# Optimization experiments

Measured on AMD Instinct MI355X. Metric: run time of the kernel, lower is better.

Reference implementation:

```python
import jax, jax.numpy as jnp
from jax import lax
import numpy as np

B, S, T, R = 64, 50, 50, 2   # batch, n_prev_sents, n_words, n_responses
V, H = 32000, 256            # vocab, hidden (= emb_size)


def gru_scan(xs, h0, Wih, Whh, bih, bhh):
    """Torch-style GRU over xs [T, N, I]; returns (outs [T,N,H], h_last [N,H])."""
    gi_all = jnp.einsum('tni,gi->tng', xs, Wih) + bih  # input gates precomputed
    def step(h, gi):
        gh = h @ Whh.T + bhh
        ir, iz, inn = jnp.split(gi, 3, -1)
        hr, hz, hn = jnp.split(gh, 3, -1)
        r = jax.nn.sigmoid(ir + hr)
        z = jax.nn.sigmoid(iz + hz)
        n = jnp.tanh(inn + r * hn)
        h = (1.0 - z) * n + z * h
        return h, h
    h_last, outs = lax.scan(step, h0, gi_all)
    return outs, h_last


def agent_tables():
    # replicates get_agent_emb: np.random.seed(1), one fresh uniform table per batch
    np.random.seed(1)
    return jnp.asarray(np.stack([np.random.uniform(0, 1, (S + 1, H)) for _ in range(B)]).astype(np.float32))


def setup_inputs() -> dict:
    key = jax.random.key(0)
    ks = jax.random.split(key, 24)
    k = 1.0 / np.sqrt(H)
    u = lambda kk, shape: jax.random.uniform(kk, shape, jnp.float32, -k, k)
    inp = {
        'context': jax.random.randint(ks[0], (B, S, T), 0, V, jnp.int32),
        'response': jax.random.randint(ks[1], (B, R, T), 0, V, jnp.int32),
        'spk_agents': jax.random.randint(ks[2], (B, S), 0, S + 1, jnp.int32),
        'emb_utter': jax.random.normal(ks[3], (V, H), jnp.float32) * 0.1,
        'emb_resp': jax.random.normal(ks[4], (V, H), jnp.float32) * 0.1,
        'utter_Wih': u(ks[5], (3 * H, H)), 'utter_Whh': u(ks[6], (3 * H, H)),
        'utter_bih': u(ks[7], (3 * H,)), 'utter_bhh': u(ks[8], (3 * H,)),
        'ctx_Wih': u(ks[9], (3 * H, 2 * H)), 'ctx_Whh': u(ks[10], (3 * H, H)),
        'ctx_bih': u(ks[11], (3 * H,)), 'ctx_bhh': u(ks[12], (3 * H,)),
        'resp_Wih': u(ks[13], (3 * H, H)), 'resp_Whh': u(ks[14], (3 * H, H)),
        'resp_bih': u(ks[15], (3 * H,)), 'resp_bhh': u(ks[16], (3 * H,)),
        'spk_Wih': u(ks[17], (3 * H, H)), 'spk_Whh': u(ks[18], (3 * H, H)),
        'spk_bih': u(ks[19], (3 * H,)), 'spk_bhh': u(ks[20], (3 * H,)),
    }
    return inp


def forward(context, response, spk_agents, emb_utter, emb_resp,
            utter_Wih, utter_Whh, utter_bih, utter_bhh,
            ctx_Wih, ctx_Whh, ctx_bih, ctx_bhh,
            resp_Wih, resp_Whh, resp_bih, resp_bhh,
            spk_Wih, spk_Whh, spk_bih, spk_bhh):
    # ---- utterance encoder: all B*S utterances batched through one GRU ----
    xu = emb_utter[context.reshape(B * S, T)]                 # [B*S, T, H]
    xu = jnp.transpose(xu, (1, 0, 2))                         # [T, B*S, H]
    _, hu = gru_scan(xu, jnp.zeros((B * S, H), jnp.float32),
                     utter_Wih, utter_Whh, utter_bih, utter_bhh)
    utter_hidden = hu.reshape(B, S, H).transpose(1, 0, 2)     # [S, B, H]

    # ---- agent embeddings (per-batch random tables, gathered by speaker id) ----
    tables = agent_tables()                                   # [B, S+1, H] constant
    agent_emb = jnp.take_along_axis(tables, spk_agents[:, :, None].astype(jnp.int32), axis=1)  # [B,S,H]
    agent_emb = jnp.transpose(agent_emb, (1, 0, 2))           # [S, B, H]

    # ---- context GRU over utterances ----
    ctx_in = jnp.concatenate([utter_hidden, agent_emb], axis=2)  # [S, B, 2H]
    context_output, ctx_h = gru_scan(ctx_in, jnp.zeros((B, H), jnp.float32),
                                     ctx_Wih, ctx_Whh, ctx_bih, ctx_bhh)
    context_hidden = ctx_h[None]                              # [1, B, H]

    # ---- speaker encoder: masked GRU == GRU over each speaker's subsequence ----
    sp_ids = jnp.arange(S + 1)
    active = (spk_agents[:, :, None] == sp_ids[None, None, :])  # [B, S, S+1]
    active_t = jnp.transpose(active, (1, 0, 2))                 # [S, B, S+1]
    gi_all = jnp.einsum('sbh,gh->sbg', context_output, spk_Wih) + spk_bih  # [S, B, 3H]

    def spk_step(h, inputs):
        gi, act = inputs                                        # gi [B,3H], act [B,S+1]
        gh = jnp.einsum('bsh,gh->bsg', h, spk_Whh) + spk_bhh    # [B, S+1, 3H]
        ir, iz, inn = jnp.split(gi[:, None, :], 3, -1)
        hr, hz, hn = jnp.split(gh, 3, -1)
        r = jax.nn.sigmoid(ir + hr)
        z = jax.nn.sigmoid(iz + hz)
        n = jnp.tanh(inn + r * hn)
        h_new = (1.0 - z) * n + z * h
        return jnp.where(act[:, :, None], h_new, h), None

    h_spk, _ = lax.scan(spk_step, jnp.zeros((B, S + 1, H), jnp.float32), (gi_all, active_t))
    present = active.any(axis=1)                               # [B, S+1]
    spk_emb = h_spk * present[:, :, None]                      # rows of absent speakers stay 0
    spk_emb_mask = (present & (sp_ids[None, :] > 0)).astype(jnp.float32)  # [B, S+1]

    # ---- response encoder: all B*R responses batched ----
    xr = emb_resp[response.reshape(B * R, T)]                  # [B*R, T, H]
    xr = jnp.transpose(xr, (1, 0, 2))                          # [T, B*R, H]
    outs, hr_ = gru_scan(xr, jnp.zeros((B * R, H), jnp.float32),
                         resp_Wih, resp_Whh, resp_bih, resp_bhh)
    resp_output = outs.reshape(T, B, R, H).transpose(2, 0, 1, 3)  # [R, T, B, H]
    resp_hidden = hr_.reshape(B, R, H).transpose(1, 0, 2)         # [R, B, H]

    return (context_output, context_hidden, resp_output, resp_hidden, spk_emb, spk_emb_mask)


def reference(context, response, spk_agents, emb_utter, emb_resp,
              utter_Wih, utter_Whh, utter_bih, utter_bhh,
              ctx_Wih, ctx_Whh, ctx_bih, ctx_bhh,
              resp_Wih, resp_Whh, resp_bih, resp_bhh,
              spk_Wih, spk_Whh, spk_bih, spk_bhh):
    return forward(context, response, spk_agents, emb_utter, emb_resp,
                   utter_Wih, utter_Whh, utter_bih, utter_bhh,
                   ctx_Wih, ctx_Whh, ctx_bih, ctx_bhh,
                   resp_Wih, resp_Whh, resp_bih, resp_bhh,
                   spk_Wih, spk_Whh, spk_bih, spk_bhh)
```

## Files before the change

kernel.cpp:

```cpp
#include <hip/hip_runtime.h>
#include <hip/hip_bf16.h>
#include <stdint.h>
#include <stdlib.h>
#include <math.h>

typedef __hip_bfloat16 bf16;
typedef unsigned short ushort;
typedef __attribute__((ext_vector_type(8))) short bhalf8;
typedef __attribute__((ext_vector_type(4))) float f32x4;

#define Bn 64
#define Sn 50
#define Tn 50
#define Hn 256

#define OFF_CTX_OUT   0
#define OFF_CTX_HID   819200
#define OFF_RESP_OUT  835584
#define OFF_RESP_HID  2473984
#define OFF_SPK_EMB   2506752
#define OFF_SPK_MASK  3342336

#define WS_FLAG   0u
#define WS_HU     256u
#define WS_REG    1638912u
#define RG_UTTQ   0u
#define RG_UTTSC  24576000u
#define RG_RESPGI 0u
#define RG_CO     9830400u
#define RG_GIC    13107200u
#define RG_GIS    18022400u
#define RG_TBL    22937600u
#define WS_END    26342912u

__device__ __forceinline__ float b2f_bits(unsigned int b) {
    union { unsigned int u; float f; } c; c.u = b; return c.f;
}
__device__ __forceinline__ float bf2f(ushort v) { return b2f_bits(((unsigned int)v) << 16); }
__device__ __forceinline__ ushort f2bf(float f) {
    union { float f; unsigned int u; } c; c.f = f;
    return (ushort)((c.u + 0x7fffu + ((c.u >> 16) & 1u)) >> 16);
}
template<bool BF>
__device__ __forceinline__ bhalf8 ldfrag(const void* __restrict__ p, size_t i) {
    if (BF) {
        return *(const bhalf8*)((const ushort*)p + i);
    } else {
        const float* q = (const float*)p + i;
        float4 a = *(const float4*)q;
        float4 b = *(const float4*)(q + 4);
        bhalf8 r;
        r[0] = (short)f2bf(a.x); r[1] = (short)f2bf(a.y);
        r[2] = (short)f2bf(a.z); r[3] = (short)f2bf(a.w);
        r[4] = (short)f2bf(b.x); r[5] = (short)f2bf(b.y);
        r[6] = (short)f2bf(b.z); r[7] = (short)f2bf(b.w);
        return r;
    }
}
template<bool BF>
__device__ __forceinline__ float ldw(const void* __restrict__ p, int i) {
    return BF ? bf2f(((const ushort*)p)[i]) : ((const float*)p)[i];
}
template<bool BF>
__device__ __forceinline__ void stout(void* __restrict__ out, size_t i, float v) {
    if (BF) ((ushort*)out)[i] = f2bf(v);
    else    ((float*)out)[i] = v;
}
__device__ __forceinline__ float fsigm(float x) {
    return __builtin_amdgcn_rcpf(1.f + __expf(-x));
}
__device__ __forceinline__ float ftanh(float x) {
    float e = __expf(-2.f * x);
    return (1.f - e) * __builtin_amdgcn_rcpf(1.f + e);
}

__global__ void sniff_kernel(const void* __restrict__ w, int* __restrict__ flag) {
    const unsigned int* p = (const unsigned int*)w;
    int tid = threadIdx.x;
    bool big = false;
    for (int i = tid; i < 512; i += 64) {
        float v = b2f_bits(p[i] << 16);
        if (!(fabsf(v) <= 1.0f)) big = true;
    }
    unsigned long long m = __ballot(big);
    if (tid == 0) *flag = (m == 0ull) ? 1 : 0;
}


template<bool BF>
__device__ void vocab_utt_body(
    const void* __restrict__ emb_u, const void* __restrict__ uWih,
    const void* __restrict__ ubih,
    char* __restrict__ Q, float* __restrict__ SC,
    float* bhs, float (*rmx)[16])
{
    const int tid = threadIdx.x;
    const int w = tid >> 6, l = tid & 63, quad = l >> 4, c = l & 15;

    for (int i = tid; i < 768; i += 512) bhs[i] = ldw<BF>(ubih, i);

    bhalf8 wf[3][2][8];
    #pragma unroll
    for (int g = 0; g < 3; ++g)
        #pragma unroll
        for (int ctl = 0; ctl < 2; ++ctl) {
            const int gcol = g * 256 + 32 * w + 16 * ctl + c;
            #pragma unroll
            for (int tk = 0; tk < 8; ++tk)
                wf[g][ctl][tk] = ldfrag<BF>(uWih, (size_t)gcol * 256 + 32 * tk + 8 * quad);
        }
    __syncthreads();

    for (int vt = blockIdx.x; vt < 2000; vt += gridDim.x) {
        f32x4 acc[3][2];
        #pragma unroll
        for (int g = 0; g < 3; ++g)
            #pragma unroll
            for (int ctl = 0; ctl < 2; ++ctl) {
                float b = bhs[g * 256 + 32 * w + 16 * ctl + c];
                acc[g][ctl] = (f32x4){b, b, b, b};
            }
        #pragma unroll
        for (int tk = 0; tk < 8; ++tk) {
            bhalf8 a = ldfrag<BF>(emb_u, (size_t)(vt * 16 + c) * 256 + 32 * tk + 8 * quad);
            #pragma unroll
            for (int g = 0; g < 3; ++g)
                #pragma unroll
                for (int ctl = 0; ctl < 2; ++ctl)
                    acc[g][ctl] = __builtin_amdgcn_mfma_f32_16x16x32_bf16(
                        a, wf[g][ctl][tk], acc[g][ctl], 0, 0, 0);
        }

        float mx[4];
        #pragma unroll
        for (int r = 0; r < 4; ++r) {
            float v = 0.f;
            #pragma unroll
            for (int g = 0; g < 3; ++g)
                #pragma unroll
                for (int ctl = 0; ctl < 2; ++ctl)
                    v = fmaxf(v, fabsf(acc[g][ctl][r]));
            mx[r] = v;
        }
        #pragma unroll
        for (int off = 1; off < 16; off <<= 1)
            #pragma unroll
            for (int r = 0; r < 4; ++r)
                mx[r] = fmaxf(mx[r], __shfl_xor(mx[r], off));
        if (c == 0)
            #pragma unroll
            for (int r = 0; r < 4; ++r) rmx[w][4 * quad + r] = mx[r];
        __syncthreads();

        #pragma unroll
        for (int r = 0; r < 4; ++r) {
            const int m = 4 * quad + r;
            float s = fmaxf(fmaxf(fmaxf(rmx[0][m], rmx[1][m]), fmaxf(rmx[2][m], rmx[3][m])),
                            fmaxf(fmaxf(rmx[4][m], rmx[5][m]), fmaxf(rmx[6][m], rmx[7][m])));
            float scale = s * (1.f / 127.f);
            float inv   = (s > 0.f) ? (127.f / s) : 0.f;
            #pragma unroll
            for (int g = 0; g < 3; ++g)
                #pragma unroll
                for (int ctl = 0; ctl < 2; ++ctl) {
                    int qv = __float2int_rn(acc[g][ctl][r] * inv);
                    qv = max(-127, min(127, qv));
                    Q[(size_t)(vt * 16 + m) * 768 + g * 256 + 32 * w + 16 * ctl + c] = (char)qv;
                }
            if (w == 0 && c == 0) SC[vt * 16 + m] = scale;
        }
        __syncthreads();
    }
}

__global__ __launch_bounds__(512, 1) void vocab_utt_kernel(
    const void* emb_u, const void* uWih, const void* ubih,
    char* Q, float* SC, const int* flag)
{
    __shared__ float bhs[768];
    __shared__ float rmx[8][16];
    if (*flag) vocab_utt_body<true >(emb_u, uWih, ubih, Q, SC, bhs, rmx);
    else       vocab_utt_body<false>(emb_u, uWih, ubih, Q, SC, bhs, rmx);
}

template<bool BF>
__device__ void rec_utt_body(
    const int* __restrict__ ctx_tok,
    const char* __restrict__ Q, const float* __restrict__ SC,
    const void* __restrict__ uWhh, const void* __restrict__ ubhh,
    ushort* __restrict__ H_u,
    char (*gq)[16][784], float (*gsc)[16], ushort (*hb)[16][264])
{
    const int n0 = blockIdx.x * 16;
    const int tid = threadIdx.x;
    const int w = tid >> 6, l = tid & 63, quad = l >> 4, c = l & 15;

    for (int i = tid; i < 16 * 264; i += 512) (&hb[0][0][0])[i] = 0;

    float breg[3][2];
    #pragma unroll
    for (int g = 0; g < 3; ++g)
        #pragma unroll
        for (int ctl = 0; ctl < 2; ++ctl)
            breg[g][ctl] = ldw<BF>(ubhh, g * 256 + 32 * w + 16 * ctl + c);

    bhalf8 wf[3][2][8];
    #pragma unroll
    for (int g = 0; g < 3; ++g)
        #pragma unroll
        for (int ctl = 0; ctl < 2; ++ctl) {
            const int gcol = g * 256 + 32 * w + 16 * ctl + c;
            #pragma unroll
            for (int tk = 0; tk < 8; ++tk)
                wf[g][ctl][tk] = ldfrag<BF>(uWhh, (size_t)gcol * 256 + 32 * tk + 8 * quad);
        }

    float st[2][4];
    #pragma unroll
    for (int ctl = 0; ctl < 2; ++ctl)
        #pragma unroll
        for (int r = 0; r < 4; ++r) st[ctl][r] = 0.f;

    const int pm = tid >> 5, pc = tid & 31;
    uint2 pf[3]; float psc = 0.f;
    {
        const int tok0 = ctx_tok[(n0 + pm) * Tn + 0];
        const char* src = Q + (size_t)tok0 * 768 + pc * 24;
        #pragma unroll
        for (int s = 0; s < 3; ++s) pf[s] = *(const uint2*)(src + s * 8);
        #pragma unroll
        for (int s = 0; s < 3; ++s) *(uint2*)(&gq[0][pm][pc * 24 + s * 8]) = pf[s];
        if (pc == 0) gsc[0][pm] = SC[tok0];
    }
    __syncthreads();

    int p = 0;
    for (int t = 0; t < Tn; ++t) {
        if (t < Tn - 1) {
            const int tok1 = ctx_tok[(n0 + pm) * Tn + t + 1];
            const char* src = Q + (size_t)tok1 * 768 + pc * 24;
            #pragma unroll
            for (int s = 0; s < 3; ++s) pf[s] = *(const uint2*)(src + s * 8);
            if (pc == 0) psc = SC[tok1];
        }

        f32x4 acc[3][2];
        #pragma unroll
        for (int g = 0; g < 3; ++g)
            #pragma unroll
            for (int ctl = 0; ctl < 2; ++ctl) {
                float b = breg[g][ctl];
                acc[g][ctl] = (f32x4){b, b, b, b};
            }
        #pragma unroll
        for (int tk = 0; tk < 8; ++tk) {
            bhalf8 a = *(const bhalf8*)(&hb[p][c][32 * tk + 8 * quad]);
            #pragma unroll
            for (int g = 0; g < 3; ++g)
                #pragma unroll
                for (int ctl = 0; ctl < 2; ++ctl)
                    acc[g][ctl] = __builtin_amdgcn_mfma_f32_16x16x32_bf16(
                        a, wf[g][ctl][tk], acc[g][ctl], 0, 0, 0);
        }

        #pragma unroll
        for (int ctl = 0; ctl < 2; ++ctl) {
            const int u = 32 * w + 16 * ctl + c;
            #pragma unroll
            for (int r = 0; r < 4; ++r) {
                const int m = 4 * quad + r;
                const float s = gsc[p][m];
                float gr = s * (float)(signed char)gq[p][m][u];
                float gz = s * (float)(signed char)gq[p][m][256 + u];
                float gn = s * (float)(signed char)gq[p][m][512 + u];
                float rr = fsigm(gr + acc[0][ctl][r]);
                float zz = fsigm(gz + acc[1][ctl][r]);
                float nn = ftanh(gn + rr * acc[2][ctl][r]);
                float h  = (1.f - zz) * nn + zz * st[ctl][r];
                st[ctl][r] = h;
                hb[p ^ 1][m][u] = f2bf(h);
            }
        }
        if (t < Tn - 1) {
            #pragma unroll
            for (int s = 0; s < 3; ++s) *(uint2*)(&gq[p ^ 1][pm][pc * 24 + s * 8]) = pf[s];
            if (pc == 0) gsc[p ^ 1][pm] = psc;
        }
        __syncthreads();
        p ^= 1;
    }

    #pragma unroll
    for (int ctl = 0; ctl < 2; ++ctl)
        #pragma unroll
        for (int r = 0; r < 4; ++r)
            H_u[(size_t)(n0 + 4 * quad + r) * Hn + 32 * w + 16 * ctl + c] = f2bf(st[ctl][r]);
}

__global__ __launch_bounds__(512, 1) void rec_utt_kernel(
    const int* ctx_tok, const char* Q, const float* SC,
    const void* uWhh, const void* ubhh, ushort* H_u, const int* flag)
{
    __shared__ char   gq[2][16][784];
    __shared__ float  gsc[2][16];
    __shared__ ushort hb[2][16][264];
    if (*flag) rec_utt_body<true >(ctx_tok, Q, SC, uWhh, ubhh, H_u, gq, gsc, hb);
    else       rec_utt_body<false>(ctx_tok, Q, SC, uWhh, ubhh, H_u, gq, gsc, hb);
}

template<bool BF>
__device__ void respgi_body(
    int bid,
    const int* __restrict__ rsp_tok, const void* __restrict__ emb_r,
    const void* __restrict__ rWih, const void* __restrict__ rbih,
    ushort* __restrict__ RG, float* bhs)
{
    const int tid = threadIdx.x;
    const int w = tid >> 6, l = tid & 63, quad = l >> 4, c = l & 15;

    for (int i = tid; i < 768; i += 512) bhs[i] = ldw<BF>(rbih, i);

    bhalf8 wf[3][2][8];
    #pragma unroll
    for (int g = 0; g < 3; ++g)
        #pragma unroll
        for (int ctl = 0; ctl < 2; ++ctl) {
            const int gcol = g * 256 + 32 * w + 16 * ctl + c;
            #pragma unroll
            for (int tk = 0; tk < 8; ++tk)
                wf[g][ctl][tk] = ldfrag<BF>(rWih, (size_t)gcol * 256 + 32 * tk + 8 * quad);
        }
    __syncthreads();

    const int inst = bid * 16 + c;
    const int tok  = rsp_tok[inst];

    f32x4 acc[3][2];
    #pragma unroll
    for (int g = 0; g < 3; ++g)
        #pragma unroll
        for (int ctl = 0; ctl < 2; ++ctl) {
            float b = bhs[g * 256 + 32 * w + 16 * ctl + c];
            acc[g][ctl] = (f32x4){b, b, b, b};
        }
    #pragma unroll
    for (int tk = 0; tk < 8; ++tk) {
        bhalf8 a = ldfrag<BF>(emb_r, (size_t)tok * 256 + 32 * tk + 8 * quad);
        #pragma unroll
        for (int g = 0; g < 3; ++g)
            #pragma unroll
            for (int ctl = 0; ctl < 2; ++ctl)
                acc[g][ctl] = __builtin_amdgcn_mfma_f32_16x16x32_bf16(
                    a, wf[g][ctl][tk], acc[g][ctl], 0, 0, 0);
    }
    #pragma unroll
    for (int g = 0; g < 3; ++g)
        #pragma unroll
        for (int ctl = 0; ctl < 2; ++ctl)
            #pragma unroll
            for (int r = 0; r < 4; ++r)
                RG[(size_t)(bid * 16 + 4 * quad + r) * 768
                   + g * 256 + 32 * w + 16 * ctl + c] = f2bf(acc[g][ctl][r]);
}

template<bool BF>
__device__ void rec_resp_body(
    int bid,
    const ushort* __restrict__ RG,
    const void* __restrict__ rWhh, const void* __restrict__ rbhh,
    void* __restrict__ outp,
    ushort (*gx)[16][776], ushort (*hb)[16][264])
{
    const int n0 = bid * 16;
    const int tid = threadIdx.x;
    const int w = tid >> 6, l = tid & 63, quad = l >> 4, c = l & 15;

    for (int i = tid; i < 16 * 264; i += 512) (&hb[0][0][0])[i] = 0;

    float breg[3][2];
    #pragma unroll
    for (int g = 0; g < 3; ++g)
        #pragma unroll
        for (int ctl = 0; ctl < 2; ++ctl)
            breg[g][ctl] = ldw<BF>(rbhh, g * 256 + 32 * w + 16 * ctl + c);

    bhalf8 wf[3][2][8];
    #pragma unroll
    for (int g = 0; g < 3; ++g)
        #pragma unroll
        for (int ctl = 0; ctl < 2; ++ctl) {
            const int gcol = g * 256 + 32 * w + 16 * ctl + c;
            #pragma unroll
            for (int tk = 0; tk < 8; ++tk)
                wf[g][ctl][tk] = ldfrag<BF>(rWhh, (size_t)gcol * 256 + 32 * tk + 8 * quad);
        }

    float st[2][4];
    #pragma unroll
    for (int ctl = 0; ctl < 2; ++ctl)
        #pragma unroll
        for (int r = 0; r < 4; ++r) st[ctl][r] = 0.f;

    const int pm = tid >> 5, pc = tid & 31;
    uint4 pf[3];
    {
        const ushort* src = RG + (size_t)((n0 + pm) * Tn + 0) * 768 + pc * 24;
        #pragma unroll
        for (int s = 0; s < 3; ++s) pf[s] = *(const uint4*)(src + s * 8);
        #pragma unroll
        for (int s = 0; s < 3; ++s) *(uint4*)(&gx[0][pm][pc * 24 + s * 8]) = pf[s];
    }
    __syncthreads();

    int p = 0;
    for (int t = 0; t < Tn; ++t) {
        if (t > 0) {
            #pragma unroll
            for (int ctl = 0; ctl < 2; ++ctl) {
                const int u = 32 * w + 16 * ctl + c;
                #pragma unroll
                for (int r = 0; r < 4; ++r) {
                    const int n = n0 + 4 * quad + r, bb = n >> 1, ri = n & 1;
                    stout<BF>(outp, OFF_RESP_OUT
                              + (size_t)((ri * Tn + (t - 1)) * Bn + bb) * Hn + u,
                              st[ctl][r]);
                }
            }
        }
        if (t < Tn - 1) {
            const ushort* src = RG + (size_t)((n0 + pm) * Tn + t + 1) * 768 + pc * 24;
            #pragma unroll
            for (int s = 0; s < 3; ++s) pf[s] = *(const uint4*)(src + s * 8);
        }

        f32x4 acc[3][2];
        #pragma unroll
        for (int g = 0; g < 3; ++g)
            #pragma unroll
            for (int ctl = 0; ctl < 2; ++ctl) {
                float b = breg[g][ctl];
                acc[g][ctl] = (f32x4){b, b, b, b};
            }
        #pragma unroll
        for (int tk = 0; tk < 8; ++tk) {
            bhalf8 a = *(const bhalf8*)(&hb[p][c][32 * tk + 8 * quad]);
            #pragma unroll
            for (int g = 0; g < 3; ++g)
                #pragma unroll
                for (int ctl = 0; ctl < 2; ++ctl)
                    acc[g][ctl] = __builtin_amdgcn_mfma_f32_16x16x32_bf16(
                        a, wf[g][ctl][tk], acc[g][ctl], 0, 0, 0);
        }

        #pragma unroll
        for (int ctl = 0; ctl < 2; ++ctl) {
            const int u = 32 * w + 16 * ctl + c;
            #pragma unroll
            for (int r = 0; r < 4; ++r) {
                const int m = 4 * quad + r;
                float gr = bf2f(gx[p][m][u]);
                float gz = bf2f(gx[p][m][256 + u]);
                float gn = bf2f(gx[p][m][512 + u]);
                float rr = fsigm(gr + acc[0][ctl][r]);
                float zz = fsigm(gz + acc[1][ctl][r]);
                float nn = ftanh(gn + rr * acc[2][ctl][r]);
                float h  = (1.f - zz) * nn + zz * st[ctl][r];
                st[ctl][r] = h;
                hb[p ^ 1][m][u] = f2bf(h);
            }
        }
        if (t < Tn - 1) {
            #pragma unroll
            for (int s = 0; s < 3; ++s) *(uint4*)(&gx[p ^ 1][pm][pc * 24 + s * 8]) = pf[s];
        }
        __syncthreads();
        p ^= 1;
    }

    #pragma unroll
    for (int ctl = 0; ctl < 2; ++ctl) {
        const int u = 32 * w + 16 * ctl + c;
        #pragma unroll
        for (int r = 0; r < 4; ++r) {
            const int n = n0 + 4 * quad + r, bb = n >> 1, ri = n & 1;
            stout<BF>(outp, OFF_RESP_OUT
                      + (size_t)((ri * Tn + (Tn - 1)) * Bn + bb) * Hn + u, st[ctl][r]);
            stout<BF>(outp, OFF_RESP_HID + (size_t)(ri * Bn + bb) * Hn + u, st[ctl][r]);
        }
    }
}

template<bool BF>
__device__ void gi_ctx_body(
    int bid,
    const ushort* __restrict__ H_u, const ushort* __restrict__ tblbf,
    const int* __restrict__ spk_agents,
    const void* __restrict__ Wih, const void* __restrict__ bih,
    ushort* __restrict__ GIc, float* bhs)
{
    const int tid = threadIdx.x;
    const int w = tid >> 6, l = tid & 63, quad = l >> 4, c = l & 15;

    for (int i = tid; i < 768; i += 512) bhs[i] = ldw<BF>(bih, i);
    __syncthreads();

    const int m0 = bid * 16;
    const int m  = m0 + c, s = m >> 6, b = m & 63;
    const int a  = spk_agents[b * Sn + s];
    const ushort* arow0 = H_u   + (size_t)(b * Sn + s) * Hn;
    const ushort* arow1 = tblbf + (size_t)(b * 51 + a) * Hn;

    f32x4 acc[3][2];
    #pragma unroll
    for (int g = 0; g < 3; ++g)
        #pragma unroll
        for (int ctl = 0; ctl < 2; ++ctl) {
            float bb = bhs[g * 256 + 32 * w + 16 * ctl + c];
            acc[g][ctl] = (f32x4){bb, bb, bb, bb};
        }

    for (int half = 0; half < 2; ++half) {
        const ushort* ar = half ? arow1 : arow0;
        bhalf8 af[8];
        #pragma unroll
        for (int tk = 0; tk < 8; ++tk)
            af[tk] = *(const bhalf8*)(ar + 32 * tk + 8 * quad);
        #pragma unroll
        for (int g = 0; g < 3; ++g) {
            bhalf8 wf[2][8];
            #pragma unroll
            for (int ctl = 0; ctl < 2; ++ctl) {
                const int gcol = g * 256 + 32 * w + 16 * ctl + c;
                #pragma unroll
                for (int tk = 0; tk < 8; ++tk)
                    wf[ctl][tk] = ldfrag<BF>(Wih,
                        (size_t)gcol * 512 + half * 256 + 32 * tk + 8 * quad);
            }
            #pragma unroll
            for (int tk = 0; tk < 8; ++tk)
                #pragma unroll
                for (int ctl = 0; ctl < 2; ++ctl)
                    acc[g][ctl] = __builtin_amdgcn_mfma_f32_16x16x32_bf16(
                        af[tk], wf[ctl][tk], acc[g][ctl], 0, 0, 0);
        }
    }

    #pragma unroll
    for (int g = 0; g < 3; ++g)
        #pragma unroll
        for (int ctl = 0; ctl < 2; ++ctl)
            #pragma unroll
            for (int r = 0; r < 4; ++r)
                GIc[(size_t)(m0 + 4 * quad + r) * 768
                    + g * 256 + 32 * w + 16 * ctl + c] = f2bf(acc[g][ctl][r]);
}

__global__ __launch_bounds__(512, 1) void gates2_kernel(
    const int* rsp_tok, const void* emb_r, const void* rWih, const void* rbih,
    ushort* RG,
    const ushort* H_u, const ushort* tblbf, const int* spk_agents,
    const void* cWih, const void* cbih, ushort* GIc, const int* flag)
{
    __shared__ float bhs[768];
    if (blockIdx.x < 400) {
        if (*flag) respgi_body<true >(blockIdx.x, rsp_tok, emb_r, rWih, rbih, RG, bhs);
        else       respgi_body<false>(blockIdx.x, rsp_tok, emb_r, rWih, rbih, RG, bhs);
    } else {
        const int bid = blockIdx.x - 400;
        if (*flag) gi_ctx_body<true >(bid, H_u, tblbf, spk_agents, cWih, cbih, GIc, bhs);
        else       gi_ctx_body<false>(bid, H_u, tblbf, spk_agents, cWih, cbih, GIc, bhs);
    }
}

template<bool BF>
__device__ void ctx_rec_body(
    int bid,
    const ushort* __restrict__ GIc,
    const void* __restrict__ Whh, const void* __restrict__ bhh,
    float* __restrict__ CO, void* __restrict__ outp,
    ushort (*gx)[16][776], ushort (*hb)[16][264])
{
    const int n0 = bid * 16;
    const int tid = threadIdx.x;
    const int w = tid >> 6, l = tid & 63, quad = l >> 4, c = l & 15;

    for (int i = tid; i < 16 * 264; i += 512) (&hb[0][0][0])[i] = 0;

    float breg[3][2];
    #pragma unroll
    for (int g = 0; g < 3; ++g)
        #pragma unroll
        for (int ctl = 0; ctl < 2; ++ctl)
            breg[g][ctl] = ldw<BF>(bhh, g * 256 + 32 * w + 16 * ctl + c);

    bhalf8 wf[3][2][8];
    #pragma unroll
    for (int g = 0; g < 3; ++g)
        #pragma unroll
        for (int ctl = 0; ctl < 2; ++ctl) {
            const int gcol = g * 256 + 32 * w + 16 * ctl + c;
            #pragma unroll
            for (int tk = 0; tk < 8; ++tk)
                wf[g][ctl][tk] = ldfrag<BF>(Whh, (size_t)gcol * 256 + 32 * tk + 8 * quad);
        }

    float st[2][4];
    #pragma unroll
    for (int ctl = 0; ctl < 2; ++ctl)
        #pragma unroll
        for (int r = 0; r < 4; ++r) st[ctl][r] = 0.f;

    const int pm = tid >> 5, pc = tid & 31;
    uint4 pf[3];
    {
        const ushort* src = GIc + (size_t)(0 * Bn + n0 + pm) * 768 + pc * 24;
        #pragma unroll
        for (int s = 0; s < 3; ++s) pf[s] = *(const uint4*)(src + s * 8);
        #pragma unroll
        for (int s = 0; s < 3; ++s) *(uint4*)(&gx[0][pm][pc * 24 + s * 8]) = pf[s];
    }
    __syncthreads();

    int p = 0;
    for (int t = 0; t < Sn; ++t) {
        if (t > 0) {
            #pragma unroll
            for (int ctl = 0; ctl < 2; ++ctl) {
                const int u = 32 * w + 16 * ctl + c;
                #pragma unroll
                for (int r = 0; r < 4; ++r) {
                    const size_t gri = (size_t)((t - 1) * Bn + n0 + 4 * quad + r);
                    CO[gri * Hn + u] = st[ctl][r];
                    stout<BF>(outp, OFF_CTX_OUT + gri * Hn + u, st[ctl][r]);
                }
            }
        }
        if (t < Sn - 1) {
            const ushort* src = GIc + (size_t)((t + 1) * Bn + n0 + pm) * 768 + pc * 24;
            #pragma unroll
            for (int s = 0; s < 3; ++s) pf[s] = *(const uint4*)(src + s * 8);
        }

        f32x4 acc[3][2];
        #pragma unroll
        for (int g = 0; g < 3; ++g)
            #pragma unroll
            for (int ctl = 0; ctl < 2; ++ctl) {
                float b = breg[g][ctl];
                acc[g][ctl] = (f32x4){b, b, b, b};
            }
        #pragma unroll
        for (int tk = 0; tk < 8; ++tk) {
            bhalf8 a = *(const bhalf8*)(&hb[p][c][32 * tk + 8 * quad]);
            #pragma unroll
            for (int g = 0; g < 3; ++g)
                #pragma unroll
                for (int ctl = 0; ctl < 2; ++ctl)
                    acc[g][ctl] = __builtin_amdgcn_mfma_f32_16x16x32_bf16(
                        a, wf[g][ctl][tk], acc[g][ctl], 0, 0, 0);
        }

        #pragma unroll
        for (int ctl = 0; ctl < 2; ++ctl) {
            const int u = 32 * w + 16 * ctl + c;
            #pragma unroll
            for (int r = 0; r < 4; ++r) {
                const int m = 4 * quad + r;
                float gr = bf2f(gx[p][m][u]);
                float gz = bf2f(gx[p][m][256 + u]);
                float gn = bf2f(gx[p][m][512 + u]);
                float rr = fsigm(gr + acc[0][ctl][r]);
                float zz = fsigm(gz + acc[1][ctl][r]);
                float nn = ftanh(gn + rr * acc[2][ctl][r]);
                float h  = (1.f - zz) * nn + zz * st[ctl][r];
                st[ctl][r] = h;
                hb[p ^ 1][m][u] = f2bf(h);
            }
        }
        if (t < Sn - 1) {
            #pragma unroll
            for (int s = 0; s < 3; ++s) *(uint4*)(&gx[p ^ 1][pm][pc * 24 + s * 8]) = pf[s];
        }
        __syncthreads();
        p ^= 1;
    }

    #pragma unroll
    for (int ctl = 0; ctl < 2; ++ctl) {
        const int u = 32 * w + 16 * ctl + c;
        #pragma unroll
        for (int r = 0; r < 4; ++r) {
            const int m = 4 * quad + r;
            const size_t gri = (size_t)((Sn - 1) * Bn + n0 + m);
            CO[gri * Hn + u] = st[ctl][r];
            stout<BF>(outp, OFF_CTX_OUT + gri * Hn + u, st[ctl][r]);
            stout<BF>(outp, OFF_CTX_HID + (size_t)(n0 + m) * Hn + u, st[ctl][r]);
        }
    }
}

__global__ __launch_bounds__(512, 1) void rec2_kernel(
    const ushort* GIc, const void* cWhh, const void* cbhh, float* CO,
    const ushort* RG, const void* rWhh, const void* rbhh,
    void* outp, const int* flag)
{
    __shared__ ushort gx[2][16][776];
    __shared__ ushort hb[2][16][264];
    if (blockIdx.x < 4) {
        if (*flag) ctx_rec_body<true >(blockIdx.x, GIc, cWhh, cbhh, CO, outp, gx, hb);
        else       ctx_rec_body<false>(blockIdx.x, GIc, cWhh, cbhh, CO, outp, gx, hb);
    } else {
        const int bid = blockIdx.x - 4;
        if (*flag) rec_resp_body<true >(bid, RG, rWhh, rbhh, outp, gx, hb);
        else       rec_resp_body<false>(bid, RG, rWhh, rbhh, outp, gx, hb);
    }
}

template<bool BF>
__device__ void gi_spk_body(
    const float* __restrict__ CO,
    const void* __restrict__ Wih, const void* __restrict__ bih,
    ushort* __restrict__ GIs, float* bhs)
{
    const int tid = threadIdx.x;
    const int w = tid >> 6, l = tid & 63, quad = l >> 4, c = l & 15;

    for (int i = tid; i < 768; i += 512) bhs[i] = ldw<BF>(bih, i);

    bhalf8 wf[3][2][8];
    #pragma unroll
    for (int g = 0; g < 3; ++g)
        #pragma unroll
        for (int ctl = 0; ctl < 2; ++ctl) {
            const int gcol = g * 256 + 32 * w + 16 * ctl + c;
            #pragma unroll
            for (int tk = 0; tk < 8; ++tk)
                wf[g][ctl][tk] = ldfrag<BF>(Wih, (size_t)gcol * 256 + 32 * tk + 8 * quad);
        }
    __syncthreads();

    f32x4 acc[3][2];
    #pragma unroll
    for (int g = 0; g < 3; ++g)
        #pragma unroll
        for (int ctl = 0; ctl < 2; ++ctl) {
            float b = bhs[g * 256 + 32 * w + 16 * ctl + c];
            acc[g][ctl] = (f32x4){b, b, b, b};
        }
    #pragma unroll
    for (int tk = 0; tk < 8; ++tk) {
        bhalf8 a = ldfrag<false>(CO, (size_t)(blockIdx.x * 16 + c) * 256 + 32 * tk + 8 * quad);
        #pragma unroll
        for (int g = 0; g < 3; ++g)
            #pragma unroll
            for (int ctl = 0; ctl < 2; ++ctl)
                acc[g][ctl] = __builtin_amdgcn_mfma_f32_16x16x32_bf16(
                    a, wf[g][ctl][tk], acc[g][ctl], 0, 0, 0);
    }
    #pragma unroll
    for (int g = 0; g < 3; ++g)
        #pragma unroll
        for (int ctl = 0; ctl < 2; ++ctl)
            #pragma unroll
            for (int r = 0; r < 4; ++r)
                GIs[(size_t)(blockIdx.x * 16 + 4 * quad + r) * 768
                    + g * 256 + 32 * w + 16 * ctl + c] = f2bf(acc[g][ctl][r]);
}

__global__ __launch_bounds__(512, 1) void gi_spk_kernel(
    const float* CO, const void* Wih, const void* bih, ushort* GIs, const int* flag)
{
    __shared__ float bhs[768];
    if (*flag) gi_spk_body<true >(CO, Wih, bih, GIs, bhs);
    else       gi_spk_body<false>(CO, Wih, bih, GIs, bhs);
}

#define SSTR 264
template<bool BF>
__device__ void spk_rec_body(
    const ushort* __restrict__ GIs,
    const void* __restrict__ Whh, const void* __restrict__ bhh,
    const int* __restrict__ spk_agents,
    void* __restrict__ outp,
    ushort* S , ushort (*gx)[776], int* pres , float* bhs)
{
    const int b0 = blockIdx.x * 4;
    const int tid = threadIdx.x;
    const int w = tid >> 6, l = tid & 63, quad = l >> 4, c = l & 15;

    for (int i = tid; i < 768; i += 512) bhs[i] = ldw<BF>(bhh, i);
    for (int i = tid; i < 4 * 51 * SSTR; i += 512) S[i] = 0;
    for (int i = tid; i < 4 * 51; i += 512) pres[i] = 0;

    bhalf8 wf[3][2][8];
    #pragma unroll
    for (int g = 0; g < 3; ++g)
        #pragma unroll
        for (int ctl = 0; ctl < 2; ++ctl) {
            const int gcol = g * 256 + 32 * w + 16 * ctl + c;
            #pragma unroll
            for (int tk = 0; tk < 8; ++tk)
                wf[g][ctl][tk] = ldfrag<BF>(Whh, (size_t)gcol * 256 + 32 * tk + 8 * quad);
        }

    const int prow = (tid & 255) >> 6;
    const int pseg = tid & 63;
    uint2 pf[3];
    if (tid < 256) {
        const ushort* src = GIs + (size_t)(0 * Bn + b0 + prow) * 768 + pseg * 12;
        #pragma unroll
        for (int s = 0; s < 3; ++s) pf[s] = *(const uint2*)(src + s * 4);
        #pragma unroll
        for (int s = 0; s < 3; ++s) *(uint2*)(&gx[prow][pseg * 12 + s * 4]) = pf[s];
    }
    __syncthreads();

    for (int t = 0; t < Sn; ++t) {
        const int va = (c < 4) ? spk_agents[(b0 + c) * Sn + t] : 0;
        const int mb = (c < 4) ? c : 0;

        if (tid < 256 && t < Sn - 1) {
            const ushort* src = GIs + (size_t)((t + 1) * Bn + b0 + prow) * 768 + pseg * 12;
            #pragma unroll
            for (int s = 0; s < 3; ++s) pf[s] = *(const uint2*)(src + s * 4);
        }

        f32x4 acc[3][2];
        #pragma unroll
        for (int g = 0; g < 3; ++g)
            #pragma unroll
            for (int ctl = 0; ctl < 2; ++ctl) {
                float b = bhs[g * 256 + 32 * w + 16 * ctl + c];
                acc[g][ctl] = (f32x4){b, b, b, b};
            }
        const ushort* srow = &S[(mb * 51 + va) * SSTR];
        #pragma unroll
        for (int tk = 0; tk < 8; ++tk) {
            bhalf8 a = *(const bhalf8*)(srow + 32 * tk + 8 * quad);
            #pragma unroll
            for (int g = 0; g < 3; ++g)
                #pragma unroll
                for (int ctl = 0; ctl < 2; ++ctl)
                    acc[g][ctl] = __builtin_amdgcn_mfma_f32_16x16x32_bf16(
                        a, wf[g][ctl][tk], acc[g][ctl], 0, 0, 0);
        }
        __syncthreads();

        if (quad == 0) {
            int vv[4];
            #pragma unroll
            for (int r = 0; r < 4; ++r) vv[r] = spk_agents[(b0 + r) * Sn + t];
            #pragma unroll
            for (int ctl = 0; ctl < 2; ++ctl) {
                const int u = 32 * w + 16 * ctl + c;
                #pragma unroll
                for (int r = 0; r < 4; ++r) {
                    ushort* sp = &S[(r * 51 + vv[r]) * SSTR + u];
                    float gr = bf2f(gx[r][u]);
                    float gz = bf2f(gx[r][256 + u]);
                    float gn = bf2f(gx[r][512 + u]);
                    float hprev = bf2f(*sp);
                    float rr = fsigm(gr + acc[0][ctl][r]);
                    float zz = fsigm(gz + acc[1][ctl][r]);
                    float nn = ftanh(gn + rr * acc[2][ctl][r]);
                    float h  = (1.f - zz) * nn + zz * hprev;
                    *sp = f2bf(h);
                }
            }
        }
        if (tid < 4) pres[tid * 51 + spk_agents[(b0 + tid) * Sn + t]] = 1;
        __syncthreads();

        if (tid < 256 && t < Sn - 1) {
            #pragma unroll
            for (int s = 0; s < 3; ++s) *(uint2*)(&gx[prow][pseg * 12 + s * 4]) = pf[s];
        }
    }
    __syncthreads();

    for (int idx = tid; idx < 4 * 51 * 256; idx += 512) {
        const int mb2 = idx / (51 * 256);
        const int rem = idx - mb2 * (51 * 256);
        const int v = rem >> 8, u = rem & 255;
        float val = bf2f(S[(mb2 * 51 + v) * SSTR + u]);
        stout<BF>(outp, OFF_SPK_EMB + (size_t)((b0 + mb2) * 51 + v) * Hn + u, val);
    }
    for (int idx = tid; idx < 4 * 51; idx += 512) {
        const int mb2 = idx / 51, v = idx - mb2 * 51;
        stout<BF>(outp, OFF_SPK_MASK + (size_t)((b0 + mb2) * 51 + v),
                  (pres[mb2 * 51 + v] && v > 0) ? 1.f : 0.f);
    }
}

__global__ __launch_bounds__(512, 1) void spk_rec_kernel(
    const ushort* GIs, const void* Whh, const void* bhh,
    const int* spk_agents, void* outp, const int* flag)
{
    __shared__ ushort S[4 * 51 * SSTR];
    __shared__ ushort gx[4][776];
    __shared__ int    pres[4 * 51];
    __shared__ float  bhs[768];
    if (*flag) spk_rec_body<true >(GIs, Whh, bhh, spk_agents, outp, S, gx, pres, bhs);
    else       spk_rec_body<false>(GIs, Whh, bhh, spk_agents, outp, S, gx, pres, bhs);
}

namespace {
inline uint16_t host_f2bf(float f) {
    union { float f; uint32_t u; } c; c.f = f;
    return (uint16_t)((c.u + 0x7fffu + ((c.u >> 16) & 1u)) >> 16);
}
struct MT19937 {
    uint32_t mt[624]; int mti;
    void seed(uint32_t s) {
        mt[0] = s;
        for (int i = 1; i < 624; ++i)
            mt[i] = 1812433253u * (mt[i - 1] ^ (mt[i - 1] >> 30)) + (uint32_t)i;
        mti = 624;
    }
    uint32_t next() {
        if (mti >= 624) {
            for (int i = 0; i < 624; ++i) {
                uint32_t y = (mt[i] & 0x80000000u) | (mt[(i + 1) % 624] & 0x7fffffffu);
                mt[i] = mt[(i + 397) % 624] ^ (y >> 1) ^ ((y & 1u) ? 0x9908b0dfu : 0u);
            }
            mti = 0;
        }
        uint32_t y = mt[mti++];
        y ^= y >> 11; y ^= (y << 7) & 0x9d2c5680u; y ^= (y << 15) & 0xefc60000u; y ^= y >> 18;
        return y;
    }
    double rd() {
        uint32_t a = next() >> 5, b = next() >> 6;
        return (a * 67108864.0 + b) / 9007199254740992.0;
    }
};

uint16_t* get_host_tables() {
    static uint16_t* p = [] {
        void* q = nullptr;
        if (hipHostMalloc(&q, 835584 * sizeof(uint16_t), hipHostMallocDefault) != hipSuccess)
            q = malloc(835584 * sizeof(uint16_t));
        uint16_t* h = (uint16_t*)q;
        MT19937 g; g.seed(1u);
        for (int i = 0; i < 835584; ++i)
            h[i] = host_f2bf((float)g.rd());
        return h;
    }();
    return p;
}
}

extern "C" void kernel_launch(void* const* d_in, const int* in_sizes, int n_in,
                              void* d_out, int out_size, void* d_ws, size_t ws_size,
                              hipStream_t stream)
{
    const int* ctx_tok    = (const int*)d_in[0];
    const int* rsp_tok    = (const int*)d_in[1];
    const int* spk_agents = (const int*)d_in[2];
    const void* emb_u = d_in[3];
    const void* emb_r = d_in[4];
    const void* uWih = d_in[5],  *uWhh = d_in[6],  *ubih = d_in[7],  *ubhh = d_in[8];
    const void* cWih = d_in[9],  *cWhh = d_in[10], *cbih = d_in[11], *cbhh = d_in[12];
    const void* rWih = d_in[13], *rWhh = d_in[14], *rbih = d_in[15], *rbhh = d_in[16];
    const void* sWih = d_in[17], *sWhh = d_in[18], *sbih = d_in[19], *sbhh = d_in[20];
    (void)in_sizes; (void)n_in; (void)out_size; (void)ws_size;

    char* ws  = (char*)d_ws;
    char* reg = ws + WS_REG;
    int*      flag = (int*)(ws + WS_FLAG);
    ushort*   H_u  = (ushort*)(ws + WS_HU);
    char*     UQ   = (char*)(reg + RG_UTTQ);
    float*    USC  = (float*)(reg + RG_UTTSC);
    ushort*   RG   = (ushort*)(reg + RG_RESPGI);
    float*    CO   = (float*)(reg + RG_CO);
    ushort*   GIc  = (ushort*)(reg + RG_GIC);
    ushort*   GIs  = (ushort*)(reg + RG_GIS);
    ushort*   tbl  = (ushort*)(reg + RG_TBL);
    void*     out  = d_out;

    sniff_kernel<<<1, 64, 0, stream>>>(uWih, flag);

    vocab_utt_kernel<<<250, 512, 0, stream>>>(emb_u, uWih, ubih, UQ, USC, flag);
    rec_utt_kernel<<<200, 512, 0, stream>>>(ctx_tok, UQ, USC, uWhh, ubhh, H_u, flag);

    hipMemcpyAsync(tbl, get_host_tables(), 835584 * sizeof(uint16_t),
                   hipMemcpyHostToDevice, stream);

    gates2_kernel<<<600, 512, 0, stream>>>(rsp_tok, emb_r, rWih, rbih, RG,
                                           H_u, tbl, spk_agents, cWih, cbih, GIc, flag);

    rec2_kernel<<<12, 512, 0, stream>>>(GIc, cWhh, cbhh, CO,
                                        RG, rWhh, rbhh, out, flag);

    gi_spk_kernel<<<200, 512, 0, stream>>>(CO, sWih, sbih, GIs, flag);
    spk_rec_kernel<<<16, 512, 0, stream>>>(GIs, sWhh, sbhh, spk_agents, out, flag);
}
```

Measured before the change: 1.244 ms.

## Prefetch recurrent gate inputs directly into LDS with global_load_lds

In the utterance, response, context and speaker GRU recurrence kernels, the next-step gate-input rows are now fetched with direct global-to-LDS loads into a double buffer. This replaces loading into registers and then writing to shared memory after the step's math. The speaker kernel gains a second gx buffer so its prefetch no longer has to wait for the post-barrier copy. The utterance kernel also precomputes all per-token scales for every timestep into LDS up front. The aim is to cut register pressure and LDS store instructions on the serial critical path. The risk is that correctness depends on the compiler placing the right wait counts on the asynchronous LDS writes before the barriers.

```diff
diff --git a/kernel.cpp b/kernel.cpp
--- a/kernel.cpp
+++ b/kernel.cpp
@@ -40,6 +40,11 @@
 __device__ __forceinline__ ushort f2bf(float f) {
     union { float f; unsigned int u; } c; c.f = f;
     return (ushort)((c.u + 0x7fffu + ((c.u >> 16) & 1u)) >> 16);
+}
+__device__ __forceinline__ void gld_lds16(const void* g, void* l) {
+    __builtin_amdgcn_global_load_lds(
+        (const __attribute__((address_space(1))) void*)g,
+        (__attribute__((address_space(3))) void*)l, 16, 0, 0);
 }
 template<bool BF>
 __device__ __forceinline__ bhalf8 ldfrag(const void* __restrict__ p, size_t i) {
@@ -189,13 +194,17 @@
     const char* __restrict__ Q, const float* __restrict__ SC,
     const void* __restrict__ uWhh, const void* __restrict__ ubhh,
     ushort* __restrict__ H_u,
-    char (*gq)[16][784], float (*gsc)[16], ushort (*hb)[16][264])
+    char (*gq)[16][784], float* gsc_all , ushort (*hb)[16][264])
 {
     const int n0 = blockIdx.x * 16;
     const int tid = threadIdx.x;
     const int w = tid >> 6, l = tid & 63, quad = l >> 4, c = l & 15;
 
     for (int i = tid; i < 16 * 264; i += 512) (&hb[0][0][0])[i] = 0;
+    for (int i = tid; i < Tn * 16; i += 512) {
+        const int t = i >> 4, m = i & 15;
+        gsc_all[i] = SC[ctx_tok[(n0 + m) * Tn + t]];
+    }
 
     float breg[3][2];
     #pragma unroll
@@ -221,27 +230,25 @@
         #pragma unroll
         for (int r = 0; r < 4; ++r) st[ctl][r] = 0.f;
 
-    const int pm = tid >> 5, pc = tid & 31;
-    uint2 pf[3]; float psc = 0.f;
-    {
-        const int tok0 = ctx_tok[(n0 + pm) * Tn + 0];
-        const char* src = Q + (size_t)tok0 * 768 + pc * 24;
-        #pragma unroll
-        for (int s = 0; s < 3; ++s) pf[s] = *(const uint2*)(src + s * 8);
-        #pragma unroll
-        for (int s = 0; s < 3; ++s) *(uint2*)(&gq[0][pm][pc * 24 + s * 8]) = pf[s];
-        if (pc == 0) gsc[0][pm] = SC[tok0];
+    #pragma unroll
+    for (int k = 0; k < 2; ++k) {
+        const int m = 2 * w + k;
+        const int tok = ctx_tok[(n0 + m) * Tn + 0];
+        if (l < 48)
+            gld_lds16(Q + (size_t)tok * 768 + l * 16, &gq[0][m][0]);
     }
     __syncthreads();
 
     int p = 0;
     for (int t = 0; t < Tn; ++t) {
         if (t < Tn - 1) {
-            const int tok1 = ctx_tok[(n0 + pm) * Tn + t + 1];
-            const char* src = Q + (size_t)tok1 * 768 + pc * 24;
-            #pragma unroll
-            for (int s = 0; s < 3; ++s) pf[s] = *(const uint2*)(src + s * 8);
-            if (pc == 0) psc = SC[tok1];
+            #pragma unroll
+            for (int k = 0; k < 2; ++k) {
+                const int m = 2 * w + k;
+                const int tok = ctx_tok[(n0 + m) * Tn + t + 1];
+                if (l < 48)
+                    gld_lds16(Q + (size_t)tok * 768 + l * 16, &gq[p ^ 1][m][0]);
+            }
         }
 
         f32x4 acc[3][2];
@@ -269,7 +276,7 @@
             #pragma unroll
             for (int r = 0; r < 4; ++r) {
                 const int m = 4 * quad + r;
-                const float s = gsc[p][m];
+                const float s = gsc_all[t * 16 + m];
                 float gr = s * (float)(signed char)gq[p][m][u];
                 float gz = s * (float)(signed char)gq[p][m][256 + u];
                 float gn = s * (float)(signed char)gq[p][m][512 + u];
@@ -281,11 +288,6 @@
                 hb[p ^ 1][m][u] = f2bf(h);
             }
         }
-        if (t < Tn - 1) {
-            #pragma unroll
-            for (int s = 0; s < 3; ++s) *(uint2*)(&gq[p ^ 1][pm][pc * 24 + s * 8]) = pf[s];
-            if (pc == 0) gsc[p ^ 1][pm] = psc;
-        }
         __syncthreads();
         p ^= 1;
     }
@@ -301,11 +303,11 @@
     const int* ctx_tok, const char* Q, const float* SC,
     const void* uWhh, const void* ubhh, ushort* H_u, const int* flag)
 {
-    __shared__ char   gq[2][16][784];
-    __shared__ float  gsc[2][16];
-    __shared__ ushort hb[2][16][264];
-    if (*flag) rec_utt_body<true >(ctx_tok, Q, SC, uWhh, ubhh, H_u, gq, gsc, hb);
-    else       rec_utt_body<false>(ctx_tok, Q, SC, uWhh, ubhh, H_u, gq, gsc, hb);
+    __shared__ __align__(16) char   gq[2][16][784];
+    __shared__ float  gsc_all[Tn * 16];
+    __shared__ __align__(16) ushort hb[2][16][264];
+    if (*flag) rec_utt_body<true >(ctx_tok, Q, SC, uWhh, ubhh, H_u, gq, gsc_all, hb);
+    else       rec_utt_body<false>(ctx_tok, Q, SC, uWhh, ubhh, H_u, gq, gsc_all, hb);
 }
 
 template<bool BF>
@@ -401,19 +403,30 @@
         #pragma unroll
         for (int r = 0; r < 4; ++r) st[ctl][r] = 0.f;
 
-    const int pm = tid >> 5, pc = tid & 31;
-    uint4 pf[3];
-    {
-        const ushort* src = RG + (size_t)((n0 + pm) * Tn + 0) * 768 + pc * 24;
-        #pragma unroll
-        for (int s = 0; s < 3; ++s) pf[s] = *(const uint4*)(src + s * 8);
-        #pragma unroll
-        for (int s = 0; s < 3; ++s) *(uint4*)(&gx[0][pm][pc * 24 + s * 8]) = pf[s];
+    #pragma unroll
+    for (int k = 0; k < 2; ++k) {
+        const int m = 2 * w + k;
+        const ushort* src = RG + (size_t)((n0 + m) * Tn + 0) * 768;
+        if (l < 48) {
+            gld_lds16(src + l * 8,       &gx[0][m][0]);
+            gld_lds16(src + 384 + l * 8, &gx[0][m][384]);
+        }
     }
     __syncthreads();
 
     int p = 0;
     for (int t = 0; t < Tn; ++t) {
+        if (t < Tn - 1) {
+            #pragma unroll
+            for (int k = 0; k < 2; ++k) {
+                const int m = 2 * w + k;
+                const ushort* src = RG + (size_t)((n0 + m) * Tn + t + 1) * 768;
+                if (l < 48) {
+                    gld_lds16(src + l * 8,       &gx[p ^ 1][m][0]);
+                    gld_lds16(src + 384 + l * 8, &gx[p ^ 1][m][384]);
+                }
+            }
+        }
         if (t > 0) {
             #pragma unroll
             for (int ctl = 0; ctl < 2; ++ctl) {
@@ -426,11 +439,6 @@
                               st[ctl][r]);
                 }
             }
-        }
-        if (t < Tn - 1) {
-            const ushort* src = RG + (size_t)((n0 + pm) * Tn + t + 1) * 768 + pc * 24;
-            #pragma unroll
-            for (int s = 0; s < 3; ++s) pf[s] = *(const uint4*)(src + s * 8);
         }
 
         f32x4 acc[3][2];
@@ -469,10 +477,6 @@
                 hb[p ^ 1][m][u] = f2bf(h);
             }
         }
-        if (t < Tn - 1) {
-            #pragma unroll
-            for (int s = 0; s < 3; ++s) *(uint4*)(&gx[p ^ 1][pm][pc * 24 + s * 8]) = pf[s];
-        }
         __syncthreads();
         p ^= 1;
     }
@@ -610,19 +614,30 @@
         #pragma unroll
         for (int r = 0; r < 4; ++r) st[ctl][r] = 0.f;
 
-    const int pm = tid >> 5, pc = tid & 31;
-    uint4 pf[3];
-    {
-        const ushort* src = GIc + (size_t)(0 * Bn + n0 + pm) * 768 + pc * 24;
-        #pragma unroll
-        for (int s = 0; s < 3; ++s) pf[s] = *(const uint4*)(src + s * 8);
-        #pragma unroll
-        for (int s = 0; s < 3; ++s) *(uint4*)(&gx[0][pm][pc * 24 + s * 8]) = pf[s];
+    #pragma unroll
+    for (int k = 0; k < 2; ++k) {
+        const int m = 2 * w + k;
+        const ushort* src = GIc + (size_t)(0 * Bn + n0 + m) * 768;
+        if (l < 48) {
+            gld_lds16(src + l * 8,       &gx[0][m][0]);
+            gld_lds16(src + 384 + l * 8, &gx[0][m][384]);
+        }
     }
     __syncthreads();
 
     int p = 0;
     for (int t = 0; t < Sn; ++t) {
+        if (t < Sn - 1) {
+            #pragma unroll
+            for (int k = 0; k < 2; ++k) {
+                const int m = 2 * w + k;
+                const ushort* src = GIc + (size_t)((t + 1) * Bn + n0 + m) * 768;
+                if (l < 48) {
+                    gld_lds16(src + l * 8,       &gx[p ^ 1][m][0]);
+                    gld_lds16(src + 384 + l * 8, &gx[p ^ 1][m][384]);
+                }
+            }
+        }
         if (t > 0) {
             #pragma unroll
             for (int ctl = 0; ctl < 2; ++ctl) {
@@ -634,11 +649,6 @@
                     stout<BF>(outp, OFF_CTX_OUT + gri * Hn + u, st[ctl][r]);
                 }
             }
-        }
-        if (t < Sn - 1) {
-            const ushort* src = GIc + (size_t)((t + 1) * Bn + n0 + pm) * 768 + pc * 24;
-            #pragma unroll
-            for (int s = 0; s < 3; ++s) pf[s] = *(const uint4*)(src + s * 8);
         }
 
         f32x4 acc[3][2];
@@ -677,10 +687,6 @@
                 hb[p ^ 1][m][u] = f2bf(h);
             }
         }
-        if (t < Sn - 1) {
-            #pragma unroll
-            for (int s = 0; s < 3; ++s) *(uint4*)(&gx[p ^ 1][pm][pc * 24 + s * 8]) = pf[s];
-        }
         __syncthreads();
         p ^= 1;
     }
@@ -704,8 +710,8 @@
     const ushort* RG, const void* rWhh, const void* rbhh,
     void* outp, const int* flag)
 {
-    __shared__ ushort gx[2][16][776];
-    __shared__ ushort hb[2][16][264];
+    __shared__ __align__(16) ushort gx[2][16][776];
+    __shared__ __align__(16) ushort hb[2][16][264];
     if (blockIdx.x < 4) {
         if (*flag) ctx_rec_body<true >(blockIdx.x, GIc, cWhh, cbhh, CO, outp, gx, hb);
         else       ctx_rec_body<false>(blockIdx.x, GIc, cWhh, cbhh, CO, outp, gx, hb);
@@ -782,7 +788,7 @@
     const void* __restrict__ Whh, const void* __restrict__ bhh,
     const int* __restrict__ spk_agents,
     void* __restrict__ outp,
-    ushort* S , ushort (*gx)[776], int* pres , float* bhs)
+    ushort* S , ushort (*gx)[4][776], int* pres , float* bhs)
 {
     const int b0 = blockIdx.x * 4;
     const int tid = threadIdx.x;
@@ -803,26 +809,22 @@
                 wf[g][ctl][tk] = ldfrag<BF>(Whh, (size_t)gcol * 256 + 32 * tk + 8 * quad);
         }
 
-    const int prow = (tid & 255) >> 6;
-    const int pseg = tid & 63;
-    uint2 pf[3];
-    if (tid < 256) {
-        const ushort* src = GIs + (size_t)(0 * Bn + b0 + prow) * 768 + pseg * 12;
-        #pragma unroll
-        for (int s = 0; s < 3; ++s) pf[s] = *(const uint2*)(src + s * 4);
-        #pragma unroll
-        for (int s = 0; s < 3; ++s) *(uint2*)(&gx[prow][pseg * 12 + s * 4]) = pf[s];
+    {
+        const int row = w >> 1, ch = w & 1;
+        const ushort* src = GIs + (size_t)(0 * Bn + b0 + row) * 768 + ch * 384;
+        if (l < 48) gld_lds16(src + l * 8, &gx[0][row][ch * 384]);
     }
     __syncthreads();
 
+    int p = 0;
     for (int t = 0; t < Sn; ++t) {
         const int va = (c < 4) ? spk_agents[(b0 + c) * Sn + t] : 0;
         const int mb = (c < 4) ? c : 0;
 
-        if (tid < 256 && t < Sn - 1) {
-            const ushort* src = GIs + (size_t)((t + 1) * Bn + b0 + prow) * 768 + pseg * 12;
-            #pragma unroll
-            for (int s = 0; s < 3; ++s) pf[s] = *(const uint2*)(src + s * 4);
+        if (t < Sn - 1) {
+            const int row = w >> 1, ch = w & 1;
+            const ushort* src = GIs + (size_t)((t + 1) * Bn + b0 + row) * 768 + ch * 384;
+            if (l < 48) gld_lds16(src + l * 8, &gx[p ^ 1][row][ch * 384]);
         }
 
         f32x4 acc[3][2];
@@ -856,9 +858,9 @@
                 #pragma unroll
                 for (int r = 0; r < 4; ++r) {
                     ushort* sp = &S[(r * 51 + vv[r]) * SSTR + u];
-                    float gr = bf2f(gx[r][u]);
-                    float gz = bf2f(gx[r][256 + u]);
-                    float gn = bf2f(gx[r][512 + u]);
+                    float gr = bf2f(gx[p][r][u]);
+                    float gz = bf2f(gx[p][r][256 + u]);
+                    float gn = bf2f(gx[p][r][512 + u]);
                     float hprev = bf2f(*sp);
                     float rr = fsigm(gr + acc[0][ctl][r]);
                     float zz = fsigm(gz + acc[1][ctl][r]);
@@ -870,11 +872,7 @@
         }
         if (tid < 4) pres[tid * 51 + spk_agents[(b0 + tid) * Sn + t]] = 1;
         __syncthreads();
-
-        if (tid < 256 && t < Sn - 1) {
-            #pragma unroll
-            for (int s = 0; s < 3; ++s) *(uint2*)(&gx[prow][pseg * 12 + s * 4]) = pf[s];
-        }
+        p ^= 1;
     }
     __syncthreads();
 
@@ -896,8 +894,8 @@
     const ushort* GIs, const void* Whh, const void* bhh,
     const int* spk_agents, void* outp, const int* flag)
 {
-    __shared__ ushort S[4 * 51 * SSTR];
-    __shared__ ushort gx[4][776];
+    __shared__ __align__(16) ushort S[4 * 51 * SSTR];
+    __shared__ __align__(16) ushort gx[2][4][776];
     __shared__ int    pres[4 * 51];
     __shared__ float  bhs[768];
     if (*flag) spk_rec_body<true >(GIs, Whh, bhh, spk_agents, outp, S, gx, pres, bhs);
```

New measurement: 1.236 ms. No clear change (-0.6%).
